# Performance work log

Hardware: AMD Instinct MI355X
Metric: run time of the kernel (lower is better)

## Reference

```python
import jax, jax.numpy as jnp
import numpy as np

B, N, DIM, H, DH, PD = 2, 1024, 768, 8, 64, 4
EPS = 1e-8


def setup_inputs() -> dict:
    key = jax.random.key(0)
    ks = jax.random.split(key, 12)
    w = lambda k, shp: jax.random.normal(k, shp, dtype=jnp.float32) * 0.02
    return {
        "x": jax.random.normal(ks[0], (B, N, DIM), dtype=jnp.float32),
        "rotations": jax.random.normal(ks[1], (B, N, 3, 3), dtype=jnp.float32),
        "translations": jax.random.normal(ks[2], (B, N, 3), dtype=jnp.float32),
        "W_sq": w(ks[3], (H * DH, DIM)),
        "W_sk": w(ks[4], (H * DH, DIM)),
        "W_sv": w(ks[5], (H * DH, DIM)),
        "W_pq": w(ks[6], (H * PD * 3, DIM)),
        "W_pk": w(ks[7], (H * PD * 3, DIM)),
        "W_pv": w(ks[8], (H * PD * 3, DIM)),
        "point_weights": jax.random.normal(ks[9], (H,), dtype=jnp.float32),
        "W_out": w(ks[10], (DIM, H * (DH + PD * 4))),
        "b_out": jax.random.normal(ks[11], (DIM,), dtype=jnp.float32) * 0.02,
    }


def reference(x, rotations, translations, W_sq, W_sk, W_sv, W_pq, W_pk, W_pv, point_weights, W_out, b_out):
    b, n, _ = x.shape
    h, dh, pd = H, DH, PD
    scalar_scale = (2 * dh) ** -0.5           # num_attn_logits=2
    point_scale = (2 * pd * (9 / 2)) ** -0.5

    # scalar q/k/v: [b,h,n,dh]
    qs = (x @ W_sq.T).reshape(b, n, h, dh).transpose(0, 2, 1, 3)
    ks = (x @ W_sk.T).reshape(b, n, h, dh).transpose(0, 2, 1, 3)
    vs = (x @ W_sv.T).reshape(b, n, h, dh).transpose(0, 2, 1, 3)

    # point q/k/v: [b,h,n,pd,3]
    qp = (x @ W_pq.T).reshape(b, n, h, pd, 3).transpose(0, 2, 1, 3, 4)
    kp = (x @ W_pk.T).reshape(b, n, h, pd, 3).transpose(0, 2, 1, 3, 4)
    vp = (x @ W_pv.T).reshape(b, n, h, pd, 3).transpose(0, 2, 1, 3, 4)

    t = translations[:, None, :, None, :]  # [b,1,n,1,3]
    # global-frame points: p_c = sum_r R[n,c,r] * p[d,r] + t
    qp = jnp.einsum('bncr,bhndr->bhndc', rotations, qp) + t
    kp = jnp.einsum('bncr,bhndr->bhndc', rotations, kp) + t
    vp = jnp.einsum('bncr,bhndr->bhndc', rotations, vp) + t

    # scalar attention logits [b,h,i,j]
    logits = jnp.einsum('bhid,bhjd->bhij', qs, ks) * scalar_scale

    # point distance term: sum_{d,c} (q-k)^2 = |q|^2 + |k|^2 - 2 q.k (no [i,j,d,c] tensor)
    q2 = jnp.sum(qp ** 2, axis=(-1, -2))  # [b,h,i]
    k2 = jnp.sum(kp ** 2, axis=(-1, -2))  # [b,h,j]
    qk = jnp.einsum('bhidc,bhjdc->bhij', qp, kp)
    point_dist = q2[..., :, None] + k2[..., None, :] - 2.0 * qk

    pw = jax.nn.softplus(point_weights)[None, :, None, None]  # [1,h,1,1]
    logits = logits - 0.5 * (point_dist * pw * point_scale)

    attn = jax.nn.softmax(logits, axis=-1)

    rs = jnp.einsum('bhij,bhjd->bhid', attn, vs)          # [b,h,n,dh]
    rp = jnp.einsum('bhij,bhjdc->bhidc', attn, vp)        # [b,h,n,pd,3]
    # back to local frame: R^T (p - t)
    rp = jnp.einsum('bnrc,bhndr->bhndc', rotations, rp - t)
    rn = jnp.sqrt(jnp.sum(rp ** 2, axis=-1) + EPS)        # [b,h,n,pd]

    rs = rs.transpose(0, 2, 1, 3).reshape(b, n, h * dh)
    rp_f = rp.transpose(0, 2, 1, 3, 4).reshape(b, n, h * pd * 3)
    rn = rn.transpose(0, 2, 1, 3).reshape(b, n, h * pd)

    results = jnp.concatenate([rs, rp_f, rn], axis=-1)    # [b,n,640]
    return results @ W_out.T + b_out
```

## Files before the change

kernel.cpp:

```cpp
#include <hip/hip_runtime.h>
#include <hip/hip_bf16.h>
#include <math.h>

#define B_  2
#define N_  1024
#define DIM_ 768
#define H_  8
#define DH_ 64
#define PD_ 4
#define NPROJ 1824
#define NPAD  1920
#define BH_ (B_*H_)
#define FDIM 640

#define OFF_RS   0u
#define OFF_RP   (OFF_RS + (size_t)BH_*N_*DH_)
#define OFF_PRAW (OFF_RP + (size_t)BH_*N_*12)
#define OFF_QA   (OFF_PRAW + (size_t)B_*N_*288)
#define OFF_KA   (OFF_QA + (size_t)BH_*N_*96/2)
#define OFF_VT   (OFF_KA + (size_t)BH_*N_*96/2)
#define OFF_XB   (OFF_VT + (size_t)BH_*80*N_/2)
#define OFF_WB   (OFF_XB + (size_t)B_*N_*DIM_/2)
#define OFF_FB   OFF_XB
#define OFF_WOB  OFF_WB

typedef __attribute__((ext_vector_type(8))) short bf16x8;
typedef __attribute__((ext_vector_type(4))) float f32x4;

__device__ __forceinline__ float dot4(float4 a, float4 b) {
    return a.x*b.x + a.y*b.y + a.z*b.z + a.w*b.w;
}
__device__ __forceinline__ unsigned short f2bf(float f) {
    __hip_bfloat16 h = __float2bfloat16(f);
    return *reinterpret_cast<unsigned short*>(&h);
}

__global__ __launch_bounds__(256) void k_cvt_x(
    const float* __restrict__ x, unsigned short* __restrict__ xb)
{
    int i = blockIdx.x * 256 + threadIdx.x;
    if (i >= (B_*N_*DIM_)/4) return;
    float4 v = reinterpret_cast<const float4*>(x)[i];
    ushort4 o;
    o.x = f2bf(v.x); o.y = f2bf(v.y); o.z = f2bf(v.z); o.w = f2bf(v.w);
    reinterpret_cast<ushort4*>(xb)[i] = o;
}

__global__ __launch_bounds__(256) void k_cvt_w(
    const float* __restrict__ Wsq, const float* __restrict__ Wsk,
    const float* __restrict__ Wsv, const float* __restrict__ Wpq,
    const float* __restrict__ Wpk, const float* __restrict__ Wpv,
    unsigned short* __restrict__ wb)
{
    int i = blockIdx.x * 256 + threadIdx.x;
    if (i >= (NPAD*DIM_)/4) return;
    int row = i / (DIM_/4);
    int c4  = i % (DIM_/4);
    ushort4 o;
    if (row >= NPROJ) {
        o.x = o.y = o.z = o.w = 0;
    } else {
        const float* W;
        if      (row < 512)  W = Wsq + (size_t)row*DIM_;
        else if (row < 1024) W = Wsk + (size_t)(row-512)*DIM_;
        else if (row < 1536) W = Wsv + (size_t)(row-1024)*DIM_;
        else if (row < 1632) W = Wpq + (size_t)(row-1536)*DIM_;
        else if (row < 1728) W = Wpk + (size_t)(row-1632)*DIM_;
        else                 W = Wpv + (size_t)(row-1728)*DIM_;
        float4 v = reinterpret_cast<const float4*>(W)[c4];
        o.x = f2bf(v.x); o.y = f2bf(v.y); o.z = f2bf(v.z); o.w = f2bf(v.w);
    }
    reinterpret_cast<ushort4*>(wb)[i] = o;
}

__global__ __launch_bounds__(256) void k_cvt_wout(
    const float* __restrict__ Wout, unsigned short* __restrict__ wob)
{
    int i = blockIdx.x * 256 + threadIdx.x;
    if (i >= (DIM_*FDIM)/4) return;
    float4 v = reinterpret_cast<const float4*>(Wout)[i];
    ushort4 o;
    o.x = f2bf(v.x); o.y = f2bf(v.y); o.z = f2bf(v.z); o.w = f2bf(v.w);
    reinterpret_cast<ushort4*>(wob)[i] = o;
}

__global__ __launch_bounds__(256) void k_proj_mfma(
    const unsigned short* __restrict__ xb,
    const unsigned short* __restrict__ wb,
    float* __restrict__ ws)
{
    __shared__ unsigned short sAB[2*128*32];
    const int tid  = threadIdx.x;
    const int lane = tid & 63;
    const int wid  = tid >> 6;
    const int mt = blockIdx.x & 15;
    const int nt = blockIdx.x >> 4;
    const int row0 = mt*128;
    const int col0 = nt*128;
    const int wr = (wid >> 1)*64;
    const int wc = (wid & 1)*64;

    f32x4 acc[4][4];
    #pragma unroll
    for (int m = 0; m < 4; ++m)
        #pragma unroll
        for (int n = 0; n < 4; ++n) acc[m][n] = (f32x4){0.f,0.f,0.f,0.f};

    for (int kt = 0; kt < DIM_/32; ++kt) {
        __syncthreads();
        #pragma unroll
        for (int t = 0; t < 4; ++t) {
            int chunk = t*4 + wid;
            int tile  = chunk >> 3;
            int crow  = (chunk & 7) * 16;
            int grow  = (tile ? col0 : row0) + crow + (lane >> 2);
            const unsigned short* gsrc = (tile ? wb : xb)
                + (size_t)grow*DIM_ + kt*32 + (lane & 3)*8;
            __builtin_amdgcn_global_load_lds(
                (const __attribute__((address_space(1))) void*)gsrc,
                (__attribute__((address_space(3))) void*)(sAB + chunk*512),
                16, 0, 0);
        }
        __syncthreads();

        bf16x8 a[4], b[4];
        #pragma unroll
        for (int m = 0; m < 4; ++m)
            a[m] = *reinterpret_cast<const bf16x8*>(
                sAB + ((wr + m*16 + (lane & 15))*32 + (lane >> 4)*8));
        #pragma unroll
        for (int n = 0; n < 4; ++n)
            b[n] = *reinterpret_cast<const bf16x8*>(
                sAB + 128*32 + ((wc + n*16 + (lane & 15))*32 + (lane >> 4)*8));
        #pragma unroll
        for (int m = 0; m < 4; ++m)
            #pragma unroll
            for (int n = 0; n < 4; ++n)
                acc[m][n] = __builtin_amdgcn_mfma_f32_16x16x32_bf16(
                    a[m], b[n], acc[m][n], 0, 0, 0);
    }

    unsigned short* qa = (unsigned short*)(ws + OFF_QA);
    unsigned short* ka = (unsigned short*)(ws + OFF_KA);
    unsigned short* vt = (unsigned short*)(ws + OFF_VT);
    float* praw = ws + OFF_PRAW;
    const float ss = 0.08838834764831845f;

    #pragma unroll
    for (int n = 0; n < 4; ++n) {
        int o = col0 + wc + n*16 + (lane & 15);
        if (o >= NPROJ) continue;
        #pragma unroll
        for (int m = 0; m < 4; ++m) {
            #pragma unroll
            for (int j = 0; j < 4; ++j) {
                int r = row0 + wr + m*16 + (lane >> 4)*4 + j;
                int bb = r >> 10, nn = r & (N_-1);
                float v = acc[m][n][j];
                if (o < 512) {
                    int h = o >> 6, c = o & 63;
                    qa[((size_t)(bb*H_ + h)*N_ + nn)*96 + c] = f2bf(v*ss);
                } else if (o < 1024) {
                    int oo = o - 512; int h = oo >> 6, c = oo & 63;
                    ka[((size_t)(bb*H_ + h)*N_ + nn)*96 + c] = f2bf(v);
                } else if (o < 1536) {
                    int oo = o - 1024; int h = oo >> 6, c = oo & 63;
                    vt[((size_t)(bb*H_ + h)*80 + c)*N_ + nn] = f2bf(v);
                } else {
                    praw[(size_t)r*288 + (o - 1536)] = v;
                }
            }
        }
    }
}

__global__ __launch_bounds__(128) void k_prep(
    const float* __restrict__ rot_g,
    const float* __restrict__ trans_g,
    const float* __restrict__ pw_g,
    float* __restrict__ ws)
{
    __shared__ float R[9], T[3];
    __shared__ float rot[3][8][4][3];
    __shared__ float p2[2][8][4];
    __shared__ float q2t[8], k2t[8], coefs[8];
    const int tid = threadIdx.x;
    const int row = blockIdx.x;
    const int b = row >> 10, n = row & (N_-1);

    if (tid < 9)  R[tid] = rot_g[(size_t)row*9 + tid];
    if (tid >= 9 && tid < 12) T[tid-9] = trans_g[(size_t)row*3 + (tid-9)];
    if (tid >= 16 && tid < 24) {
        float pw = pw_g[tid-16];
        coefs[tid-16] = 0.5f * log1pf(__expf(pw)) * (1.0f/6.0f);
    }
    __syncthreads();
    if (tid < 96) {
        int which = tid >> 5, idx = tid & 31;
        int h = idx >> 2, pd = idx & 3;
        const float* p = ws + OFF_PRAW + (size_t)row*288 + which*96 + h*12 + pd*3;
        float px = p[0], py = p[1], pz = p[2];
        float c0 = R[0]*px + R[1]*py + R[2]*pz + T[0];
        float c1 = R[3]*px + R[4]*py + R[5]*pz + T[1];
        float c2 = R[6]*px + R[7]*py + R[8]*pz + T[2];
        rot[which][h][pd][0] = c0;
        rot[which][h][pd][1] = c1;
        rot[which][h][pd][2] = c2;
        if (which < 2) p2[which][h][pd] = c0*c0 + c1*c1 + c2*c2;
    }
    __syncthreads();
    if (tid < 16) {
        int w = tid >> 3, h = tid & 7;
        float s = p2[w][h][0] + p2[w][h][1] + p2[w][h][2] + p2[w][h][3];
        if (w) k2t[h] = s; else q2t[h] = s;
    }
    __syncthreads();

    unsigned short* qa = (unsigned short*)(ws + OFF_QA);
    unsigned short* ka = (unsigned short*)(ws + OFF_KA);
    unsigned short* vt = (unsigned short*)(ws + OFF_VT);

    for (int i = tid; i < 256; i += 128) {
        int h = i >> 5, c = i & 31;
        float qv, kv;
        if (c < 12)      { qv = rot[0][h][c/3][c%3] * 2.f * coefs[h]; kv = rot[1][h][c/3][c%3]; }
        else if (c == 12){ qv = q2t[h];  kv = -coefs[h]; }
        else if (c == 13){ qv = 1.f;     kv = -coefs[h]*k2t[h]; }
        else             { qv = 0.f;     kv = 0.f; }
        size_t base = ((size_t)(b*H_ + h)*N_ + n)*96 + 64 + c;
        qa[base] = f2bf(qv);
        ka[base] = f2bf(kv);
    }
    {
        int h = tid >> 4, r = tid & 15;
        float vv = (r < 12) ? rot[2][h][r/3][r%3] : 0.f;
        vt[((size_t)(b*H_ + h)*80 + 64 + r)*N_ + n] = f2bf(vv);
    }
}

#define VPAD 72
__global__ __launch_bounds__(256) void k_attn_mfma(
    const unsigned short* __restrict__ qa_g,
    const unsigned short* __restrict__ ka_g,
    const unsigned short* __restrict__ vt_g,
    float* __restrict__ ws)
{
    __shared__ unsigned short sP[4][16*VPAD];
    __shared__ float sMrg[32*80];
    __shared__ float sML[32*2];

    const int tid  = threadIdx.x;
    const int lane = tid & 63;
    const int wid  = tid >> 6;
    const int lo = lane & 15;
    const int hi = lane >> 4;
    const int bh = blockIdx.x >> 5;
    const int qt = blockIdx.x & 31;
    const int q0 = qt * 32;
    const int mrow = (wid & 1) * 16;
    const int half = wid >> 1;

    const unsigned short* Qa = qa_g + (size_t)bh*N_*96;
    const unsigned short* Ka = ka_g + (size_t)bh*N_*96;
    const unsigned short* Vt = vt_g + (size_t)bh*80*N_;

    bf16x8 qfr[3];
    {
        int qrow = q0 + mrow + lo;
        #pragma unroll
        for (int c = 0; c < 3; ++c)
            qfr[c] = *reinterpret_cast<const bf16x8*>(
                Qa + (size_t)qrow*96 + c*32 + hi*8);
    }

    f32x4 acc[5];
    #pragma unroll
    for (int d = 0; d < 5; ++d) acc[d] = (f32x4){0.f,0.f,0.f,0.f};
    float m[4] = {-1e30f,-1e30f,-1e30f,-1e30f};
    float l[4] = {0.f,0.f,0.f,0.f};

    for (int it = 0; it < 8; ++it) {
        const int j0 = (half*8 + it)*64;

        f32x4 s[4];
        #pragma unroll
        for (int t = 0; t < 4; ++t) s[t] = (f32x4){0.f,0.f,0.f,0.f};
        #pragma unroll
        for (int c = 0; c < 3; ++c) {
            bf16x8 kb[4];
            #pragma unroll
            for (int t = 0; t < 4; ++t)
                kb[t] = *reinterpret_cast<const bf16x8*>(
                    Ka + (size_t)(j0 + t*16 + lo)*96 + c*32 + hi*8);
            #pragma unroll
            for (int t = 0; t < 4; ++t)
                s[t] = __builtin_amdgcn_mfma_f32_16x16x32_bf16(qfr[c], kb[t], s[t], 0, 0, 0);
        }

        float scl[4];
        #pragma unroll
        for (int r = 0; r < 4; ++r) {
            float v = fmaxf(fmaxf(s[0][r], s[1][r]), fmaxf(s[2][r], s[3][r]));
            v = fmaxf(v, __shfl_xor(v, 1));
            v = fmaxf(v, __shfl_xor(v, 2));
            v = fmaxf(v, __shfl_xor(v, 4));
            v = fmaxf(v, __shfl_xor(v, 8));
            float mn = fmaxf(m[r], v);
            scl[r] = __expf(m[r] - mn);
            m[r] = mn;
        }
        float ps[4] = {0.f,0.f,0.f,0.f};
        #pragma unroll
        for (int t = 0; t < 4; ++t) {
            #pragma unroll
            for (int r = 0; r < 4; ++r) {
                float p = __expf(s[t][r] - m[r]);
                ps[r] += p;
                sP[wid][(hi*4 + r)*VPAD + t*16 + lo] = f2bf(p);
            }
        }
        #pragma unroll
        for (int r = 0; r < 4; ++r) {
            float v = ps[r];
            v += __shfl_xor(v, 1);
            v += __shfl_xor(v, 2);
            v += __shfl_xor(v, 4);
            v += __shfl_xor(v, 8);
            l[r] = l[r]*scl[r] + v;
        }
        #pragma unroll
        for (int d = 0; d < 5; ++d)
            #pragma unroll
            for (int r = 0; r < 4; ++r) acc[d][r] *= scl[r];

        #pragma unroll
        for (int kk = 0; kk < 2; ++kk) {
            bf16x8 pa = *reinterpret_cast<const bf16x8*>(
                &sP[wid][lo*VPAD + kk*32 + hi*8]);
            #pragma unroll
            for (int dt = 0; dt < 5; ++dt) {
                bf16x8 vb = *reinterpret_cast<const bf16x8*>(
                    Vt + (size_t)(dt*16 + lo)*N_ + j0 + kk*32 + hi*8);
                acc[dt] = __builtin_amdgcn_mfma_f32_16x16x32_bf16(pa, vb, acc[dt], 0, 0, 0);
            }
        }
    }

    __syncthreads();
    if (half == 1) {
        #pragma unroll
        for (int r = 0; r < 4; ++r) {
            int rl = mrow + hi*4 + r;
            #pragma unroll
            for (int dt = 0; dt < 5; ++dt)
                sMrg[rl*80 + dt*16 + lo] = acc[dt][r];
            if (lo == 0) { sML[rl*2] = m[r]; sML[rl*2+1] = l[r]; }
        }
    }
    __syncthreads();
    if (half == 0) {
        float* ws_rs = ws + OFF_RS + (size_t)bh*N_*DH_;
        float* ws_rp = ws + OFF_RP + (size_t)bh*N_*12;
        #pragma unroll
        for (int r = 0; r < 4; ++r) {
            int rl = mrow + hi*4 + r;
            float m2 = sML[rl*2], l2 = sML[rl*2+1];
            float mm = fmaxf(m[r], m2);
            float f1 = __expf(m[r] - mm), f2 = __expf(m2 - mm);
            float inv = 1.f / (l[r]*f1 + l2*f2);
            int i = q0 + rl;
            #pragma unroll
            for (int dt = 0; dt < 5; ++dt) {
                float val = (acc[dt][r]*f1 + sMrg[rl*80 + dt*16 + lo]*f2) * inv;
                int d = dt*16 + lo;
                if (d < 64)
                    ws_rs[(size_t)i*DH_ + d] = val;
                else if (d - 64 < 12)
                    ws_rp[(size_t)i*12 + (d - 64)] = val;
            }
        }
    }
}

__global__ __launch_bounds__(256) void k_fin_prep(
    const float* __restrict__ rotations,
    const float* __restrict__ translations,
    const float* __restrict__ ws,
    unsigned short* __restrict__ fb)
{
    __shared__ float sF[8][FDIM];
    const int tid = threadIdx.x;
    const int row0 = blockIdx.x * 8;
    const int b = row0 >> 10;
    const float* ws_rs = ws + OFF_RS;
    const float* ws_rp = ws + OFF_RP;

    for (int i = tid; i < 8*512; i += 256) {
        int r = i >> 9, f = i & 511;
        int h = f >> 6, c = f & 63;
        int n = (row0 & (N_-1)) + r;
        sF[r][f] = ws_rs[(((size_t)(b*H_ + h))*N_ + n)*DH_ + c];
    }
    {
        int r = tid >> 5;
        int idx = tid & 31;
        int h = idx >> 2, pd = idx & 3;
        int row = row0 + r;
        int n = row & (N_-1);
        const float* rp = ws_rp + (((size_t)(b*H_ + h))*N_ + n)*12 + pd*3;
        const float* R = rotations + (size_t)row*9;
        const float* T = translations + (size_t)row*3;
        float d0 = rp[0] - T[0], d1 = rp[1] - T[1], d2 = rp[2] - T[2];
        float l0 = R[0]*d0 + R[3]*d1 + R[6]*d2;
        float l1 = R[1]*d0 + R[4]*d1 + R[7]*d2;
        float l2 = R[2]*d0 + R[5]*d1 + R[8]*d2;
        sF[r][512 + h*12 + pd*3 + 0] = l0;
        sF[r][512 + h*12 + pd*3 + 1] = l1;
        sF[r][512 + h*12 + pd*3 + 2] = l2;
        sF[r][608 + h*4 + pd] = sqrtf(l0*l0 + l1*l1 + l2*l2 + 1e-8f);
    }
    __syncthreads();

    #pragma unroll
    for (int r = 0; r < 8; ++r) {
        for (int f = tid; f < FDIM; f += 256) {
            fb[(size_t)(row0 + r)*FDIM + f] = f2bf(sF[r][f]);
        }
    }
}

__global__ __launch_bounds__(256) void k_out_mfma(
    const unsigned short* __restrict__ fb,
    const unsigned short* __restrict__ wob,
    const float* __restrict__ bout,
    float* __restrict__ out)
{
    __shared__ unsigned short sAB[2*128*32];
    const int tid  = threadIdx.x;
    const int lane = tid & 63;
    const int wid  = tid >> 6;
    const int mt = blockIdx.x & 15;
    const int nt = blockIdx.x >> 4;
    const int row0 = mt*128;
    const int col0 = nt*128;
    const int wr = (wid >> 1)*64;
    const int wc = (wid & 1)*64;

    f32x4 acc[4][4];
    #pragma unroll
    for (int m = 0; m < 4; ++m)
        #pragma unroll
        for (int n = 0; n < 4; ++n) acc[m][n] = (f32x4){0.f,0.f,0.f,0.f};

    for (int kt = 0; kt < FDIM/32; ++kt) {
        __syncthreads();
        #pragma unroll
        for (int t = 0; t < 4; ++t) {
            int chunk = t*4 + wid;
            int tile  = chunk >> 3;
            int crow  = (chunk & 7) * 16;
            int grow  = (tile ? col0 : row0) + crow + (lane >> 2);
            const unsigned short* gsrc = (tile ? wob : fb)
                + (size_t)grow*FDIM + kt*32 + (lane & 3)*8;
            __builtin_amdgcn_global_load_lds(
                (const __attribute__((address_space(1))) void*)gsrc,
                (__attribute__((address_space(3))) void*)(sAB + chunk*512),
                16, 0, 0);
        }
        __syncthreads();

        bf16x8 a[4], b[4];
        #pragma unroll
        for (int m = 0; m < 4; ++m)
            a[m] = *reinterpret_cast<const bf16x8*>(
                sAB + ((wr + m*16 + (lane & 15))*32 + (lane >> 4)*8));
        #pragma unroll
        for (int n = 0; n < 4; ++n)
            b[n] = *reinterpret_cast<const bf16x8*>(
                sAB + 128*32 + ((wc + n*16 + (lane & 15))*32 + (lane >> 4)*8));
        #pragma unroll
        for (int m = 0; m < 4; ++m)
            #pragma unroll
            for (int n = 0; n < 4; ++n)
                acc[m][n] = __builtin_amdgcn_mfma_f32_16x16x32_bf16(
                    a[m], b[n], acc[m][n], 0, 0, 0);
    }

    #pragma unroll
    for (int n = 0; n < 4; ++n) {
        int o = col0 + wc + n*16 + (lane & 15);
        float bo = bout[o];
        #pragma unroll
        for (int m = 0; m < 4; ++m) {
            #pragma unroll
            for (int j = 0; j < 4; ++j) {
                int r = row0 + wr + m*16 + (lane >> 4)*4 + j;
                out[(size_t)r*DIM_ + o] = acc[m][n][j] + bo;
            }
        }
    }
}

extern "C" void kernel_launch(void* const* d_in, const int* in_sizes, int n_in,
                              void* d_out, int out_size, void* d_ws, size_t ws_size,
                              hipStream_t stream) {
    const float* x            = (const float*)d_in[0];
    const float* rotations    = (const float*)d_in[1];
    const float* translations = (const float*)d_in[2];
    const float* Wsq          = (const float*)d_in[3];
    const float* Wsk          = (const float*)d_in[4];
    const float* Wsv          = (const float*)d_in[5];
    const float* Wpq          = (const float*)d_in[6];
    const float* Wpk          = (const float*)d_in[7];
    const float* Wpv          = (const float*)d_in[8];
    const float* pweights     = (const float*)d_in[9];
    const float* Wout         = (const float*)d_in[10];
    const float* bout         = (const float*)d_in[11];
    float* out = (float*)d_out;
    float* ws  = (float*)d_ws;

    unsigned short* xb  = (unsigned short*)(ws + OFF_XB);
    unsigned short* wb  = (unsigned short*)(ws + OFF_WB);
    unsigned short* qa  = (unsigned short*)(ws + OFF_QA);
    unsigned short* ka  = (unsigned short*)(ws + OFF_KA);
    unsigned short* vt  = (unsigned short*)(ws + OFF_VT);
    unsigned short* fb  = (unsigned short*)(ws + OFF_FB);
    unsigned short* wob = (unsigned short*)(ws + OFF_WOB);

    k_cvt_x<<<(B_*N_*DIM_/4 + 255)/256, 256, 0, stream>>>(x, xb);
    k_cvt_w<<<(NPAD*DIM_/4 + 255)/256, 256, 0, stream>>>(Wsq, Wsk, Wsv, Wpq, Wpk, Wpv, wb);
    k_proj_mfma<<<16*15, 256, 0, stream>>>(xb, wb, ws);
    k_prep<<<B_*N_, 128, 0, stream>>>(rotations, translations, pweights, ws);
    k_attn_mfma<<<BH_*32, 256, 0, stream>>>(qa, ka, vt, ws);
    k_cvt_wout<<<(DIM_*FDIM/4 + 255)/256, 256, 0, stream>>>(Wout, wob);
    k_fin_prep<<<B_*N_/8, 256, 0, stream>>>(rotations, translations, ws, fb);
    k_out_mfma<<<16*6, 256, 0, stream>>>(fb, wob, bout, out);
}
```

Measured before the change: 112.7 us.

## Split attention key range across four waves per query half with block swizzle

```diff
diff --git a/kernel.cpp b/kernel.cpp
--- a/kernel.cpp
+++ b/kernel.cpp
@@ -239,26 +239,30 @@
 }
 
 #define VPAD 72
-__global__ __launch_bounds__(256) void k_attn_mfma(
+#define APAD 84
+__global__ __launch_bounds__(512) void k_attn_mfma(
     const unsigned short* __restrict__ qa_g,
     const unsigned short* __restrict__ ka_g,
     const unsigned short* __restrict__ vt_g,
     float* __restrict__ ws)
 {
-    __shared__ unsigned short sP[4][16*VPAD];
-    __shared__ float sMrg[32*80];
-    __shared__ float sML[32*2];
+    __shared__ unsigned short sP[8][16*VPAD];
+    __shared__ float sAcc[3][2][16][APAD];
+    __shared__ float sML[3][2][16][2];
 
     const int tid  = threadIdx.x;
     const int lane = tid & 63;
     const int wid  = tid >> 6;
     const int lo = lane & 15;
     const int hi = lane >> 4;
-    const int bh = blockIdx.x >> 5;
-    const int qt = blockIdx.x & 31;
+    const int bid = blockIdx.x;
+    const int Lb = (bid & 7)*64 + (bid >> 3);
+    const int bh = Lb >> 5;
+    const int qt = Lb & 31;
     const int q0 = qt * 32;
-    const int mrow = (wid & 1) * 16;
-    const int half = wid >> 1;
+    const int qh = wid & 1;
+    const int kq = wid >> 1;
+    const int mrow = qh * 16;
 
     const unsigned short* Qa = qa_g + (size_t)bh*N_*96;
     const unsigned short* Ka = ka_g + (size_t)bh*N_*96;
@@ -279,8 +283,9 @@
     float m[4] = {-1e30f,-1e30f,-1e30f,-1e30f};
     float l[4] = {0.f,0.f,0.f,0.f};
 
-    for (int it = 0; it < 8; ++it) {
-        const int j0 = (half*8 + it)*64;
+    #pragma unroll 2
+    for (int it = 0; it < 4; ++it) {
+        const int j0 = (kq*4 + it)*64;
 
         f32x4 s[4];
         #pragma unroll
@@ -346,32 +351,48 @@
         }
     }
 
+    if (kq > 0) {
+        #pragma unroll
+        for (int r = 0; r < 4; ++r) {
+            int rl = hi*4 + r;
+            #pragma unroll
+            for (int dt = 0; dt < 5; ++dt)
+                sAcc[kq-1][qh][rl][dt*16 + lo] = acc[dt][r];
+            if (lo == 0) { sML[kq-1][qh][rl][0] = m[r]; sML[kq-1][qh][rl][1] = l[r]; }
+        }
+    }
     __syncthreads();
-    if (half == 1) {
-        #pragma unroll
-        for (int r = 0; r < 4; ++r) {
-            int rl = mrow + hi*4 + r;
-            #pragma unroll
-            for (int dt = 0; dt < 5; ++dt)
-                sMrg[rl*80 + dt*16 + lo] = acc[dt][r];
-            if (lo == 0) { sML[rl*2] = m[r]; sML[rl*2+1] = l[r]; }
-        }
-    }
-    __syncthreads();
-    if (half == 0) {
+    if (kq == 0) {
         float* ws_rs = ws + OFF_RS + (size_t)bh*N_*DH_;
         float* ws_rp = ws + OFF_RP + (size_t)bh*N_*12;
         #pragma unroll
         for (int r = 0; r < 4; ++r) {
-            int rl = mrow + hi*4 + r;
-            float m2 = sML[rl*2], l2 = sML[rl*2+1];
-            float mm = fmaxf(m[r], m2);
-            float f1 = __expf(m[r] - mm), f2 = __expf(m2 - mm);
-            float inv = 1.f / (l[r]*f1 + l2*f2);
-            int i = q0 + rl;
+            int rl = hi*4 + r;
+            float mp[3], lp[3];
+            float mm = m[r];
+            #pragma unroll
+            for (int p = 0; p < 3; ++p) {
+                mp[p] = sML[p][qh][rl][0];
+                lp[p] = sML[p][qh][rl][1];
+                mm = fmaxf(mm, mp[p]);
+            }
+            float f0 = __expf(m[r] - mm);
+            float Lsum = l[r]*f0;
+            float fp[3];
+            #pragma unroll
+            for (int p = 0; p < 3; ++p) {
+                fp[p] = __expf(mp[p] - mm);
+                Lsum += lp[p]*fp[p];
+            }
+            float inv = 1.f / Lsum;
+            int i = q0 + mrow + rl;
             #pragma unroll
             for (int dt = 0; dt < 5; ++dt) {
-                float val = (acc[dt][r]*f1 + sMrg[rl*80 + dt*16 + lo]*f2) * inv;
+                float val = acc[dt][r]*f0;
+                #pragma unroll
+                for (int p = 0; p < 3; ++p)
+                    val += sAcc[p][qh][rl][dt*16 + lo]*fp[p];
+                val *= inv;
                 int d = dt*16 + lo;
                 if (d < 64)
                     ws_rs[(size_t)i*DH_ + d] = val;
@@ -531,7 +552,7 @@
     k_cvt_w<<<(NPAD*DIM_/4 + 255)/256, 256, 0, stream>>>(Wsq, Wsk, Wsv, Wpq, Wpk, Wpv, wb);
     k_proj_mfma<<<16*15, 256, 0, stream>>>(xb, wb, ws);
     k_prep<<<B_*N_, 128, 0, stream>>>(rotations, translations, pweights, ws);
-    k_attn_mfma<<<BH_*32, 256, 0, stream>>>(qa, ka, vt, ws);
+    k_attn_mfma<<<BH_*32, 512, 0, stream>>>(qa, ka, vt, ws);
     k_cvt_wout<<<(DIM_*FDIM/4 + 255)/256, 256, 0, stream>>>(Wout, wob);
     k_fin_prep<<<B_*N_/8, 256, 0, stream>>>(rotations, translations, ws, fb);
     k_out_mfma<<<16*6, 256, 0, stream>>>(fb, wob, bout, out);
```

Result: faster. 104.0 us (-7.7%).
